# Kernel tuning notes

Measured on AMD Instinct MI355X. Metric: run time of the kernel, lower is better.

Reference implementation:

```python
import jax, jax.numpy as jnp
import numpy as np

B, T, C, HS = 64, 256, 2048, 128


def setup_inputs() -> dict:
    key = jax.random.key(0)
    k1, k2, k3, k4 = jax.random.split(key, 4)
    x = jax.random.normal(k1, (B, T, C), dtype=jnp.float32)
    # Dense(head_size, use_bias=False) kernels, scaled like glorot-ish init
    Wk = jax.random.normal(k2, (C, HS), dtype=jnp.float32) * (C ** -0.5)
    Wq = jax.random.normal(k3, (C, HS), dtype=jnp.float32) * (C ** -0.5)
    Wv = jax.random.normal(k4, (C, HS), dtype=jnp.float32) * (C ** -0.5)
    return {"x": x, "Wk": Wk, "Wq": Wq, "Wv": Wv}


def reference(x, Wk, Wq, Wv):
    Bn, Tn, Cn = x.shape
    k = jnp.einsum("btc,ch->bth", x, Wk)
    q = jnp.einsum("btc,ch->bth", x, Wq)
    v = jnp.einsum("btc,ch->bth", x, Wv)
    # faithful to source: scores = k @ q^T, scaled by C**-0.5 (input dim!)
    scores = jnp.einsum("bth,bsh->bts", k, q) * (Cn ** -0.5)
    causal = jnp.tril(jnp.ones((Tn, Tn), dtype=bool))  # [T, T]
    scores = jnp.where(causal, scores, -jnp.inf)
    weights = jax.nn.softmax(scores, axis=-1)
    return jnp.einsum("bts,bsh->bth", weights, v)
```

## Files before the change

### kernel.cpp

```cpp
#include <hip/hip_runtime.h>
#include <hip/hip_bf16.h>
#include <cstdint>
#include <cstddef>

#define B_  64
#define T_  256
#define C_  2048
#define HS_ 128
#define N_  384

typedef __bf16 bf16x8 __attribute__((ext_vector_type(8)));
typedef float  floatx4 __attribute__((ext_vector_type(4)));

__device__ __forceinline__ unsigned short f2bf_rne(float f) {
  union { float f; unsigned int u; } v; v.f = f;
  unsigned int r = v.u + 0x7fffu + ((v.u >> 16) & 1u);
  return (unsigned short)(r >> 16);
}
__device__ __forceinline__ unsigned short f2bf(float f) {
  union { float f; unsigned int u; } v; v.f = f;
  return (unsigned short)((v.u + 0x8000u) >> 16);
}

__device__ __forceinline__ void async_copy16(const void* g, void* l) {
  __builtin_amdgcn_global_load_lds(
      (const __attribute__((address_space(1))) unsigned int*)g,
      (__attribute__((address_space(3))) unsigned int*)l, 16, 0, 0);
}

__global__ __launch_bounds__(256) void wt_kernel(
    const float* __restrict__ Wk, const float* __restrict__ Wq,
    const float* __restrict__ Wv, unsigned short* __restrict__ Wt) {
  __shared__ float tile[32][33];
  const int w  = blockIdx.z;
  const int c0 = blockIdx.x * 32;
  const int h0 = blockIdx.y * 32;
  const float* W = (w == 0) ? Wk : (w == 1) ? Wq : Wv;
  const int tx = threadIdx.x & 31, ty = threadIdx.x >> 5;
#pragma unroll
  for (int i = 0; i < 32; i += 8)
    tile[ty + i][tx] = W[(size_t)(c0 + ty + i) * HS_ + h0 + tx];
  __syncthreads();
#pragma unroll
  for (int i = 0; i < 32; i += 8) {
    int hh = ty + i, cc = tx;
    Wt[(size_t)(w * HS_ + h0 + hh) * C_ + c0 + cc] = f2bf_rne(tile[cc][hh]);
  }
}

__global__ __launch_bounds__(256, 2) void qkv_gemm(
    const float* __restrict__ X, const unsigned short* __restrict__ Wt,
    unsigned short* __restrict__ kqv, unsigned short* __restrict__ vT) {
  __shared__ unsigned short As[2][128 * 72];
  __shared__ unsigned short Bs[2][96 * 64];

  const int tid  = threadIdx.x;
  const int wave = tid >> 6, lane = tid & 63;
  const int quad = lane >> 4, l16 = lane & 15;

  const int bid = blockIdx.x;
  const int m0  = (bid & 127) * 128;
  const int n0  = (bid >> 7) * 96;
  const int wm  = (wave >> 1) * 64;
  const int wn  = (wave & 1) * 48;

  int bsrc_n[3], bsrc_c[3], bdst[3];
#pragma unroll
  for (int r = 0; r < 3; ++r) {
    int slot = r * 256 + tid;
    int n = slot >> 3, sl = slot & 7;
    bsrc_n[r] = n; bsrc_c[r] = sl ^ (n & 7);
    bdst[r] = (r * 256 + wave * 64) * 8;
  }

  const int arow = tid >> 4;
  const int achk = tid & 15;

#pragma unroll
  for (int r = 0; r < 3; ++r)
    async_copy16(Wt + (size_t)(n0 + bsrc_n[r]) * C_ + bsrc_c[r] * 8,
                 &Bs[0][bdst[r]]);
  float4 av[8];
#pragma unroll
  for (int r = 0; r < 8; ++r)
    av[r] = *(const float4*)(X + (size_t)(m0 + arow + r * 16) * C_ + achk * 4);

  floatx4 acc[4][3] = {};

  for (int k = 0; k < 32; ++k) {
    const int cur = k & 1, nxt = cur ^ 1;
#pragma unroll
    for (int r = 0; r < 8; ++r) {
      ushort4 b4;
      b4.x = f2bf(av[r].x); b4.y = f2bf(av[r].y);
      b4.z = f2bf(av[r].z); b4.w = f2bf(av[r].w);
      *(ushort4*)&As[cur][(arow + r * 16) * 72 + achk * 4] = b4;
    }
    __syncthreads();

    if (k < 31) {
      const int kn = (k + 1) * 64;
#pragma unroll
      for (int r = 0; r < 3; ++r)
        async_copy16(Wt + (size_t)(n0 + bsrc_n[r]) * C_ + kn + bsrc_c[r] * 8,
                     &Bs[nxt][bdst[r]]);
#pragma unroll
      for (int r = 0; r < 8; ++r)
        av[r] = *(const float4*)(X + (size_t)(m0 + arow + r * 16) * C_ + kn + achk * 4);
    }

#pragma unroll
    for (int ks = 0; ks < 2; ++ks) {
      bf16x8 af[4], bfv[3];
#pragma unroll
      for (int mt = 0; mt < 4; ++mt)
        af[mt] = *(const bf16x8*)&As[cur][(wm + mt * 16 + l16) * 72 + ks * 32 + quad * 8];
#pragma unroll
      for (int nt = 0; nt < 3; ++nt) {
        int n = wn + nt * 16 + l16;
        int c = ks * 4 + quad;
        bfv[nt] = *(const bf16x8*)&Bs[cur][n * 64 + (c ^ (n & 7)) * 8];
      }
#pragma unroll
      for (int mt = 0; mt < 4; ++mt)
#pragma unroll
        for (int nt = 0; nt < 3; ++nt)
          acc[mt][nt] = __builtin_amdgcn_mfma_f32_16x16x32_bf16(
              af[mt], bfv[nt], acc[mt][nt], 0, 0, 0);
    }
  }

#pragma unroll
  for (int mt = 0; mt < 4; ++mt)
#pragma unroll
    for (int nt = 0; nt < 3; ++nt)
#pragma unroll
      for (int r = 0; r < 4; ++r) {
        int row = m0 + wm + mt * 16 + quad * 4 + r;
        int col = n0 + wn + nt * 16 + l16;
        unsigned short us = f2bf(acc[mt][nt][r]);
        kqv[(size_t)row * N_ + col] = us;
        if (col >= 256) {
          int bb = row >> 8, tt = row & 255;
          vT[(size_t)bb * HS_ * T_ + (size_t)(col - 256) * T_ + tt] = us;
        }
      }
}

__global__ __launch_bounds__(256) void attn_kernel(
    const unsigned short* __restrict__ kqv, const unsigned short* __restrict__ vT,
    float* __restrict__ out) {
  __shared__ unsigned short P[4][16 * 136];
  __shared__ float Olds[2][16][132];
  __shared__ float rs1[2][16];

  const int tid  = threadIdx.x;
  const int wave = tid >> 6, lane = tid & 63;
  const int quad = lane >> 4, l16 = lane & 15;
  const int tile = wave >> 1, par = wave & 1;
  const int tt = tile ? (15 - (int)blockIdx.x) : (int)blockIdx.x;
  const int b  = blockIdx.y;
  const int t0 = tt * 16;
  const float scale = 0.022097086912079612f;
  const unsigned short* kq = kqv + (size_t)b * T_ * N_;

  bf16x8 kf[4];
#pragma unroll
  for (int ks = 0; ks < 4; ++ks)
    kf[ks] = *(const bf16x8*)&kq[(size_t)(t0 + l16) * N_ + ks * 32 + quad * 8];

  const int n_my = ((tt + 1) + (1 - par)) >> 1;
  const int npad = (n_my + 1) & ~1;

  float rsum[4] = {0.f, 0.f, 0.f, 0.f};

  bf16x8 qf[4];
  if (n_my > 0) {
    const int st = par;
#pragma unroll
    for (int ks = 0; ks < 4; ++ks)
      qf[ks] = *(const bf16x8*)&kq[(size_t)(st * 16 + l16) * N_ + HS_ + ks * 32 + quad * 8];
  }
  for (int j = 0; j < n_my; ++j) {
    bf16x8 qn[4];
    if (j + 1 < n_my) {
      const int st = par + 2 * (j + 1);
#pragma unroll
      for (int ks = 0; ks < 4; ++ks)
        qn[ks] = *(const bf16x8*)&kq[(size_t)(st * 16 + l16) * N_ + HS_ + ks * 32 + quad * 8];
    }
    floatx4 a = {};
#pragma unroll
    for (int ks = 0; ks < 4; ++ks)
      a = __builtin_amdgcn_mfma_f32_16x16x32_bf16(kf[ks], qf[ks], a, 0, 0, 0);
    const int st = par + 2 * j;
    const int scol = st * 16 + l16;
#pragma unroll
    for (int r = 0; r < 4; ++r) {
      int trow = t0 + quad * 4 + r;
      float p = (scol <= trow) ? __expf(a[r] * scale) : 0.f;
      rsum[r] += p;
      P[wave][(quad * 4 + r) * 136 + j * 16 + l16] = f2bf(p);
    }
#pragma unroll
    for (int ks = 0; ks < 4; ++ks) qf[ks] = qn[ks];
  }
  if (npad > n_my) {
#pragma unroll
    for (int r = 0; r < 4; ++r)
      P[wave][(quad * 4 + r) * 136 + n_my * 16 + l16] = 0;
  }
#pragma unroll
  for (int m = 1; m < 16; m <<= 1)
#pragma unroll
    for (int r = 0; r < 4; ++r)
      rsum[r] += __shfl_xor(rsum[r], m, 64);

  floatx4 oacc[8] = {};
  const unsigned short* vb = vT + (size_t)b * HS_ * T_;
  const int nks = npad >> 1;
  const int sb_off = (quad >> 1);
  const int sb_lo  = (quad & 1) * 8;
  bf16x8 bv[8]; bf16x8 pa;
  if (nks > 0) {
    int st = par + 2 * (0 + sb_off);
    int sbase = st * 16 + sb_lo;
    pa = *(const bf16x8*)&P[wave][l16 * 136 + 0 * 32 + quad * 8];
#pragma unroll
    for (int nt = 0; nt < 8; ++nt)
      bv[nt] = *(const bf16x8*)&vb[(size_t)(nt * 16 + l16) * T_ + sbase];
  }
  for (int ks2 = 0; ks2 < nks; ++ks2) {
    bf16x8 bvn[8]; bf16x8 pan;
    if (ks2 + 1 < nks) {
      int jt = 2 * (ks2 + 1) + sb_off;
      int st = par + 2 * jt;
      int sbase = st * 16 + sb_lo;
      pan = *(const bf16x8*)&P[wave][l16 * 136 + (ks2 + 1) * 32 + quad * 8];
#pragma unroll
      for (int nt = 0; nt < 8; ++nt)
        bvn[nt] = *(const bf16x8*)&vb[(size_t)(nt * 16 + l16) * T_ + sbase];
    }
#pragma unroll
    for (int nt = 0; nt < 8; ++nt)
      oacc[nt] = __builtin_amdgcn_mfma_f32_16x16x32_bf16(pa, bv[nt], oacc[nt], 0, 0, 0);
    pa = pan;
#pragma unroll
    for (int nt = 0; nt < 8; ++nt) bv[nt] = bvn[nt];
  }

  if (par == 1) {
#pragma unroll
    for (int nt = 0; nt < 8; ++nt)
#pragma unroll
      for (int r = 0; r < 4; ++r)
        Olds[tile][quad * 4 + r][nt * 16 + l16] = oacc[nt][r];
    if (l16 == 0) {
#pragma unroll
      for (int r = 0; r < 4; ++r) rs1[tile][quad * 4 + r] = rsum[r];
    }
  }
  __syncthreads();
  if (par == 0) {
    float inv[4];
#pragma unroll
    for (int r = 0; r < 4; ++r)
      inv[r] = 1.f / (rsum[r] + rs1[tile][quad * 4 + r]);
    float* ob = out + ((size_t)b * T_ + t0) * HS_;
#pragma unroll
    for (int nt = 0; nt < 8; ++nt)
#pragma unroll
      for (int r = 0; r < 4; ++r) {
        int row = quad * 4 + r;
        ob[(size_t)row * HS_ + nt * 16 + l16] =
            (oacc[nt][r] + Olds[tile][row][nt * 16 + l16]) * inv[r];
      }
  }
}

extern "C" void kernel_launch(void* const* d_in, const int* in_sizes, int n_in,
                              void* d_out, int out_size, void* d_ws, size_t ws_size,
                              hipStream_t stream) {
  const float* x  = (const float*)d_in[0];
  const float* Wk = (const float*)d_in[1];
  const float* Wq = (const float*)d_in[2];
  const float* Wv = (const float*)d_in[3];
  float* out = (float*)d_out;

  char* ws = (char*)d_ws;
  unsigned short* Wt  = (unsigned short*)(ws);
  unsigned short* kqv = (unsigned short*)(ws + 1572864);
  unsigned short* vT  = (unsigned short*)(ws + 1572864 + 12582912);

  hipLaunchKernelGGL(wt_kernel, dim3(64, 4, 3), dim3(256), 0, stream, Wk, Wq, Wv, Wt);
  hipLaunchKernelGGL(qkv_gemm, dim3(512), dim3(256), 0, stream, x, Wt, kqv, vT);
  hipLaunchKernelGGL(attn_kernel, dim3(8, 64), dim3(256), 0, stream, kqv, vT, out);
}
```

Before: 241.8 us.

## Retile QKV GEMM to full-N 32-row blocks and split attention keys four ways

The QKV projection now gives each block 32 rows of x and all 384 output columns, with a K step of 32. Each x element is therefore read and converted to bf16 only once, where before it was read once per N tile. The cost is more B-tile traffic per block and a longer K loop with more barriers. The attention kernel now runs one query tile per block, with its four waves splitting the key tiles four ways and reducing partial outputs through shared memory; the explicit register prefetch of Q and V is dropped, which trades latency hiding for a simpler loop and a better-balanced grid.

```diff
diff --git a/kernel.cpp b/kernel.cpp
--- a/kernel.cpp
+++ b/kernel.cpp
@@ -51,93 +51,79 @@
 __global__ __launch_bounds__(256, 2) void qkv_gemm(
     const float* __restrict__ X, const unsigned short* __restrict__ Wt,
     unsigned short* __restrict__ kqv, unsigned short* __restrict__ vT) {
-  __shared__ unsigned short As[2][128 * 72];
-  __shared__ unsigned short Bs[2][96 * 64];
+  __shared__ unsigned short As[2][32 * 40];
+  __shared__ unsigned short Bs[2][384 * 32];
 
   const int tid  = threadIdx.x;
   const int wave = tid >> 6, lane = tid & 63;
   const int quad = lane >> 4, l16 = lane & 15;
 
-  const int bid = blockIdx.x;
-  const int m0  = (bid & 127) * 128;
-  const int n0  = (bid >> 7) * 96;
-  const int wm  = (wave >> 1) * 64;
-  const int wn  = (wave & 1) * 48;
-
-  int bsrc_n[3], bsrc_c[3], bdst[3];
-#pragma unroll
-  for (int r = 0; r < 3; ++r) {
-    int slot = r * 256 + tid;
-    int n = slot >> 3, sl = slot & 7;
-    bsrc_n[r] = n; bsrc_c[r] = sl ^ (n & 7);
+  const int m0 = blockIdx.x * 32;
+  const int wn = wave * 96;
+
+  int bn[6], bc[6], bdst[6];
+#pragma unroll
+  for (int r = 0; r < 6; ++r) {
+    int s = r * 256 + tid;
+    int n = s >> 2, c = s & 3;
+    bn[r] = n; bc[r] = c ^ (n & 3);
     bdst[r] = (r * 256 + wave * 64) * 8;
   }
 
-  const int arow = tid >> 4;
-  const int achk = tid & 15;
-
-#pragma unroll
-  for (int r = 0; r < 3; ++r)
-    async_copy16(Wt + (size_t)(n0 + bsrc_n[r]) * C_ + bsrc_c[r] * 8,
-                 &Bs[0][bdst[r]]);
-  float4 av[8];
-#pragma unroll
-  for (int r = 0; r < 8; ++r)
-    av[r] = *(const float4*)(X + (size_t)(m0 + arow + r * 16) * C_ + achk * 4);
-
-  floatx4 acc[4][3] = {};
-
-  for (int k = 0; k < 32; ++k) {
+  const int arow = tid >> 3;
+  const int achk = tid & 7;
+
+#pragma unroll
+  for (int r = 0; r < 6; ++r)
+    async_copy16(Wt + (size_t)bn[r] * C_ + bc[r] * 8, &Bs[0][bdst[r]]);
+  float4 av = *(const float4*)(X + (size_t)(m0 + arow) * C_ + achk * 4);
+
+  floatx4 acc[2][6] = {};
+
+  for (int k = 0; k < 64; ++k) {
     const int cur = k & 1, nxt = cur ^ 1;
-#pragma unroll
-    for (int r = 0; r < 8; ++r) {
+    {
       ushort4 b4;
-      b4.x = f2bf(av[r].x); b4.y = f2bf(av[r].y);
-      b4.z = f2bf(av[r].z); b4.w = f2bf(av[r].w);
-      *(ushort4*)&As[cur][(arow + r * 16) * 72 + achk * 4] = b4;
+      b4.x = f2bf(av.x); b4.y = f2bf(av.y);
+      b4.z = f2bf(av.z); b4.w = f2bf(av.w);
+      *(ushort4*)&As[cur][arow * 40 + achk * 4] = b4;
     }
     __syncthreads();
 
-    if (k < 31) {
-      const int kn = (k + 1) * 64;
-#pragma unroll
-      for (int r = 0; r < 3; ++r)
-        async_copy16(Wt + (size_t)(n0 + bsrc_n[r]) * C_ + kn + bsrc_c[r] * 8,
-                     &Bs[nxt][bdst[r]]);
-#pragma unroll
-      for (int r = 0; r < 8; ++r)
-        av[r] = *(const float4*)(X + (size_t)(m0 + arow + r * 16) * C_ + kn + achk * 4);
-    }
-
-#pragma unroll
-    for (int ks = 0; ks < 2; ++ks) {
-      bf16x8 af[4], bfv[3];
-#pragma unroll
-      for (int mt = 0; mt < 4; ++mt)
-        af[mt] = *(const bf16x8*)&As[cur][(wm + mt * 16 + l16) * 72 + ks * 32 + quad * 8];
-#pragma unroll
-      for (int nt = 0; nt < 3; ++nt) {
-        int n = wn + nt * 16 + l16;
-        int c = ks * 4 + quad;
-        bfv[nt] = *(const bf16x8*)&Bs[cur][n * 64 + (c ^ (n & 7)) * 8];
-      }
-#pragma unroll
-      for (int mt = 0; mt < 4; ++mt)
-#pragma unroll
-        for (int nt = 0; nt < 3; ++nt)
-          acc[mt][nt] = __builtin_amdgcn_mfma_f32_16x16x32_bf16(
-              af[mt], bfv[nt], acc[mt][nt], 0, 0, 0);
-    }
-  }
-
-#pragma unroll
-  for (int mt = 0; mt < 4; ++mt)
-#pragma unroll
-    for (int nt = 0; nt < 3; ++nt)
+    if (k < 63) {
+      const int kn = (k + 1) * 32;
+#pragma unroll
+      for (int r = 0; r < 6; ++r)
+        async_copy16(Wt + (size_t)bn[r] * C_ + kn + bc[r] * 8, &Bs[nxt][bdst[r]]);
+      av = *(const float4*)(X + (size_t)(m0 + arow) * C_ + kn + achk * 4);
+    }
+
+    bf16x8 af[2], bfv[6];
+#pragma unroll
+    for (int mt = 0; mt < 2; ++mt)
+      af[mt] = *(const bf16x8*)&As[cur][(mt * 16 + l16) * 40 + quad * 8];
+#pragma unroll
+    for (int nt = 0; nt < 6; ++nt) {
+      int n = wn + nt * 16 + l16;
+      int c = quad ^ (n & 3);
+      bfv[nt] = *(const bf16x8*)&Bs[cur][n * 32 + c * 8];
+    }
+#pragma unroll
+    for (int mt = 0; mt < 2; ++mt)
+#pragma unroll
+      for (int nt = 0; nt < 6; ++nt)
+        acc[mt][nt] = __builtin_amdgcn_mfma_f32_16x16x32_bf16(
+            af[mt], bfv[nt], acc[mt][nt], 0, 0, 0);
+  }
+
+#pragma unroll
+  for (int mt = 0; mt < 2; ++mt)
+#pragma unroll
+    for (int nt = 0; nt < 6; ++nt)
 #pragma unroll
       for (int r = 0; r < 4; ++r) {
-        int row = m0 + wm + mt * 16 + quad * 4 + r;
-        int col = n0 + wn + nt * 16 + l16;
+        int row = m0 + mt * 16 + quad * 4 + r;
+        int col = wn + nt * 16 + l16;
         unsigned short us = f2bf(acc[mt][nt][r]);
         kqv[(size_t)row * N_ + col] = us;
         if (col >= 256) {
@@ -150,15 +136,15 @@
 __global__ __launch_bounds__(256) void attn_kernel(
     const unsigned short* __restrict__ kqv, const unsigned short* __restrict__ vT,
     float* __restrict__ out) {
-  __shared__ unsigned short P[4][16 * 136];
-  __shared__ float Olds[2][16][132];
-  __shared__ float rs1[2][16];
+  __shared__ unsigned short P[4][16 * 72];
+  __shared__ float Olds[3][16][132];
+  __shared__ float rs1[3][16];
 
   const int tid  = threadIdx.x;
-  const int wave = tid >> 6, lane = tid & 63;
+  const int par  = tid >> 6;
+  const int lane = tid & 63;
   const int quad = lane >> 4, l16 = lane & 15;
-  const int tile = wave >> 1, par = wave & 1;
-  const int tt = tile ? (15 - (int)blockIdx.x) : (int)blockIdx.x;
+  const int tt = blockIdx.x;
   const int b  = blockIdx.y;
   const int t0 = tt * 16;
   const float scale = 0.022097086912079612f;
@@ -169,46 +155,34 @@
   for (int ks = 0; ks < 4; ++ks)
     kf[ks] = *(const bf16x8*)&kq[(size_t)(t0 + l16) * N_ + ks * 32 + quad * 8];
 
-  const int n_my = ((tt + 1) + (1 - par)) >> 1;
+  const int n_my = (tt >= par) ? (((tt - par) >> 2) + 1) : 0;
   const int npad = (n_my + 1) & ~1;
 
   float rsum[4] = {0.f, 0.f, 0.f, 0.f};
 
-  bf16x8 qf[4];
-  if (n_my > 0) {
-    const int st = par;
+  for (int j = 0; j < n_my; ++j) {
+    const int st = par + 4 * j;
+    bf16x8 qf[4];
 #pragma unroll
     for (int ks = 0; ks < 4; ++ks)
       qf[ks] = *(const bf16x8*)&kq[(size_t)(st * 16 + l16) * N_ + HS_ + ks * 32 + quad * 8];
-  }
-  for (int j = 0; j < n_my; ++j) {
-    bf16x8 qn[4];
-    if (j + 1 < n_my) {
-      const int st = par + 2 * (j + 1);
-#pragma unroll
-      for (int ks = 0; ks < 4; ++ks)
-        qn[ks] = *(const bf16x8*)&kq[(size_t)(st * 16 + l16) * N_ + HS_ + ks * 32 + quad * 8];
-    }
     floatx4 a = {};
 #pragma unroll
     for (int ks = 0; ks < 4; ++ks)
       a = __builtin_amdgcn_mfma_f32_16x16x32_bf16(kf[ks], qf[ks], a, 0, 0, 0);
-    const int st = par + 2 * j;
     const int scol = st * 16 + l16;
 #pragma unroll
     for (int r = 0; r < 4; ++r) {
       int trow = t0 + quad * 4 + r;
       float p = (scol <= trow) ? __expf(a[r] * scale) : 0.f;
       rsum[r] += p;
-      P[wave][(quad * 4 + r) * 136 + j * 16 + l16] = f2bf(p);
-    }
-#pragma unroll
-    for (int ks = 0; ks < 4; ++ks) qf[ks] = qn[ks];
+      P[par][(quad * 4 + r) * 72 + j * 16 + l16] = f2bf(p);
+    }
   }
   if (npad > n_my) {
 #pragma unroll
     for (int r = 0; r < 4; ++r)
-      P[wave][(quad * 4 + r) * 136 + n_my * 16 + l16] = 0;
+      P[par][(quad * 4 + r) * 72 + n_my * 16 + l16] = 0;
   }
 #pragma unroll
   for (int m = 1; m < 16; m <<= 1)
@@ -221,59 +195,46 @@
   const int nks = npad >> 1;
   const int sb_off = (quad >> 1);
   const int sb_lo  = (quad & 1) * 8;
-  bf16x8 bv[8]; bf16x8 pa;
-  if (nks > 0) {
-    int st = par + 2 * (0 + sb_off);
-    int sbase = st * 16 + sb_lo;
-    pa = *(const bf16x8*)&P[wave][l16 * 136 + 0 * 32 + quad * 8];
+  for (int ks2 = 0; ks2 < nks; ++ks2) {
+    const int jt = 2 * ks2 + sb_off;
+    const int st = par + 4 * jt;
+    const int sbase = st * 16 + sb_lo;
+    bf16x8 pa = *(const bf16x8*)&P[par][l16 * 72 + ks2 * 32 + quad * 8];
+#pragma unroll
+    for (int nt = 0; nt < 8; ++nt) {
+      bf16x8 bv = *(const bf16x8*)&vb[(size_t)(nt * 16 + l16) * T_ + sbase];
+      oacc[nt] = __builtin_amdgcn_mfma_f32_16x16x32_bf16(pa, bv, oacc[nt], 0, 0, 0);
+    }
+  }
+
+  if (par > 0) {
 #pragma unroll
     for (int nt = 0; nt < 8; ++nt)
-      bv[nt] = *(const bf16x8*)&vb[(size_t)(nt * 16 + l16) * T_ + sbase];
-  }
-  for (int ks2 = 0; ks2 < nks; ++ks2) {
-    bf16x8 bvn[8]; bf16x8 pan;
-    if (ks2 + 1 < nks) {
-      int jt = 2 * (ks2 + 1) + sb_off;
-      int st = par + 2 * jt;
-      int sbase = st * 16 + sb_lo;
-      pan = *(const bf16x8*)&P[wave][l16 * 136 + (ks2 + 1) * 32 + quad * 8];
-#pragma unroll
-      for (int nt = 0; nt < 8; ++nt)
-        bvn[nt] = *(const bf16x8*)&vb[(size_t)(nt * 16 + l16) * T_ + sbase];
-    }
-#pragma unroll
-    for (int nt = 0; nt < 8; ++nt)
-      oacc[nt] = __builtin_amdgcn_mfma_f32_16x16x32_bf16(pa, bv[nt], oacc[nt], 0, 0, 0);
-    pa = pan;
-#pragma unroll
-    for (int nt = 0; nt < 8; ++nt) bv[nt] = bvn[nt];
-  }
-
-  if (par == 1) {
-#pragma unroll
-    for (int nt = 0; nt < 8; ++nt)
 #pragma unroll
       for (int r = 0; r < 4; ++r)
-        Olds[tile][quad * 4 + r][nt * 16 + l16] = oacc[nt][r];
+        Olds[par - 1][quad * 4 + r][nt * 16 + l16] = oacc[nt][r];
     if (l16 == 0) {
 #pragma unroll
-      for (int r = 0; r < 4; ++r) rs1[tile][quad * 4 + r] = rsum[r];
+      for (int r = 0; r < 4; ++r) rs1[par - 1][quad * 4 + r] = rsum[r];
     }
   }
   __syncthreads();
   if (par == 0) {
     float inv[4];
 #pragma unroll
-    for (int r = 0; r < 4; ++r)
-      inv[r] = 1.f / (rsum[r] + rs1[tile][quad * 4 + r]);
+    for (int r = 0; r < 4; ++r) {
+      int row = quad * 4 + r;
+      inv[r] = 1.f / (rsum[r] + rs1[0][row] + rs1[1][row] + rs1[2][row]);
+    }
     float* ob = out + ((size_t)b * T_ + t0) * HS_;
 #pragma unroll
     for (int nt = 0; nt < 8; ++nt)
 #pragma unroll
       for (int r = 0; r < 4; ++r) {
         int row = quad * 4 + r;
-        ob[(size_t)row * HS_ + nt * 16 + l16] =
-            (oacc[nt][r] + Olds[tile][row][nt * 16 + l16]) * inv[r];
+        int col = nt * 16 + l16;
+        ob[(size_t)row * HS_ + col] =
+            (oacc[nt][r] + Olds[0][row][col] + Olds[1][row][col] + Olds[2][row][col]) * inv[r];
       }
   }
 }
@@ -294,5 +255,5 @@
 
   hipLaunchKernelGGL(wt_kernel, dim3(64, 4, 3), dim3(256), 0, stream, Wk, Wq, Wv, Wt);
   hipLaunchKernelGGL(qkv_gemm, dim3(512), dim3(256), 0, stream, x, Wt, kqv, vT);
-  hipLaunchKernelGGL(attn_kernel, dim3(8, 64), dim3(256), 0, stream, kqv, vT, out);
-}
+  hipLaunchKernelGGL(attn_kernel, dim3(16, 64), dim3(256), 0, stream, kqv, vT, out);
+}
```

Result: slower. 290.2 us (+20.0%).

## Restructure QKV GEMM tiling to 64x192 with register-staged double-buffered prefetch

Applied to the files above, without the earlier changes.

The QKV projection GEMM moves from 128x96 tiles to 64x192 tiles, so every block covers two of the three weight matrices' columns. The async global-to-LDS copies for the weights are replaced by register prefetch, with two k-steps of A and B kept in flight. The A tile also gets an XOR-swizzled LDS layout, and a hand-written lgkmcnt wait plus barrier replaces __syncthreads. This aims to hide global load latency and cut LDS bank conflicts, at the cost of more registers per thread and possible occupancy loss.

```diff
diff --git a/kernel.cpp b/kernel.cpp
--- a/kernel.cpp
+++ b/kernel.cpp
@@ -20,12 +20,6 @@
 __device__ __forceinline__ unsigned short f2bf(float f) {
   union { float f; unsigned int u; } v; v.f = f;
   return (unsigned short)((v.u + 0x8000u) >> 16);
-}
-
-__device__ __forceinline__ void async_copy16(const void* g, void* l) {
-  __builtin_amdgcn_global_load_lds(
-      (const __attribute__((address_space(1))) unsigned int*)g,
-      (__attribute__((address_space(3))) unsigned int*)l, 16, 0, 0);
 }
 
 __global__ __launch_bounds__(256) void wt_kernel(
@@ -51,89 +45,113 @@
 __global__ __launch_bounds__(256, 2) void qkv_gemm(
     const float* __restrict__ X, const unsigned short* __restrict__ Wt,
     unsigned short* __restrict__ kqv, unsigned short* __restrict__ vT) {
-  __shared__ unsigned short As[2][128 * 72];
-  __shared__ unsigned short Bs[2][96 * 64];
+  __shared__ unsigned short As[2][64 * 64];
+  __shared__ unsigned short Bs[2][192 * 64];
 
   const int tid  = threadIdx.x;
   const int wave = tid >> 6, lane = tid & 63;
   const int quad = lane >> 4, l16 = lane & 15;
 
   const int bid = blockIdx.x;
-  const int m0  = (bid & 127) * 128;
-  const int n0  = (bid >> 7) * 96;
-  const int wm  = (wave >> 1) * 64;
-  const int wn  = (wave & 1) * 48;
-
-  int bsrc_n[3], bsrc_c[3], bdst[3];
-#pragma unroll
-  for (int r = 0; r < 3; ++r) {
-    int slot = r * 256 + tid;
-    int n = slot >> 3, sl = slot & 7;
-    bsrc_n[r] = n; bsrc_c[r] = sl ^ (n & 7);
-    bdst[r] = (r * 256 + wave * 64) * 8;
-  }
-
-  const int arow = tid >> 4;
-  const int achk = tid & 15;
-
-#pragma unroll
-  for (int r = 0; r < 3; ++r)
-    async_copy16(Wt + (size_t)(n0 + bsrc_n[r]) * C_ + bsrc_c[r] * 8,
-                 &Bs[0][bdst[r]]);
-  float4 av[8];
-#pragma unroll
-  for (int r = 0; r < 8; ++r)
-    av[r] = *(const float4*)(X + (size_t)(m0 + arow + r * 16) * C_ + achk * 4);
-
-  floatx4 acc[4][3] = {};
-
-  for (int k = 0; k < 32; ++k) {
-    const int cur = k & 1, nxt = cur ^ 1;
-#pragma unroll
-    for (int r = 0; r < 8; ++r) {
-      ushort4 b4;
-      b4.x = f2bf(av[r].x); b4.y = f2bf(av[r].y);
-      b4.z = f2bf(av[r].z); b4.w = f2bf(av[r].w);
-      *(ushort4*)&As[cur][(arow + r * 16) * 72 + achk * 4] = b4;
-    }
-    __syncthreads();
-
-    if (k < 31) {
-      const int kn = (k + 1) * 64;
-#pragma unroll
-      for (int r = 0; r < 3; ++r)
-        async_copy16(Wt + (size_t)(n0 + bsrc_n[r]) * C_ + kn + bsrc_c[r] * 8,
-                     &Bs[nxt][bdst[r]]);
-#pragma unroll
-      for (int r = 0; r < 8; ++r)
-        av[r] = *(const float4*)(X + (size_t)(m0 + arow + r * 16) * C_ + kn + achk * 4);
-    }
-
-#pragma unroll
-    for (int ks = 0; ks < 2; ++ks) {
-      bf16x8 af[4], bfv[3];
-#pragma unroll
-      for (int mt = 0; mt < 4; ++mt)
-        af[mt] = *(const bf16x8*)&As[cur][(wm + mt * 16 + l16) * 72 + ks * 32 + quad * 8];
-#pragma unroll
-      for (int nt = 0; nt < 3; ++nt) {
-        int n = wn + nt * 16 + l16;
-        int c = ks * 4 + quad;
-        bfv[nt] = *(const bf16x8*)&Bs[cur][n * 64 + (c ^ (n & 7)) * 8];
-      }
-#pragma unroll
-      for (int mt = 0; mt < 4; ++mt)
-#pragma unroll
-        for (int nt = 0; nt < 3; ++nt)
-          acc[mt][nt] = __builtin_amdgcn_mfma_f32_16x16x32_bf16(
-              af[mt], bfv[nt], acc[mt][nt], 0, 0, 0);
-    }
-  }
-
-#pragma unroll
-  for (int mt = 0; mt < 4; ++mt)
-#pragma unroll
-    for (int nt = 0; nt < 3; ++nt)
+  const int m0  = (bid & 255) * 64;
+  const int n0  = (bid >> 8) * 192;
+  const int wm  = (wave >> 1) * 32;
+  const int wn  = (wave & 1) * 96;
+
+  int arow[4], achk[4], aoff[4];
+#pragma unroll
+  for (int r = 0; r < 4; ++r) {
+    int s = r * 256 + tid;
+    arow[r] = s >> 4; achk[r] = s & 15;
+    aoff[r] = arow[r] * 64 + (((achk[r] >> 1) ^ (arow[r] & 7)) << 3) + ((achk[r] & 1) << 2);
+  }
+  int bn[6], bc[6], boff[6];
+#pragma unroll
+  for (int r = 0; r < 6; ++r) {
+    int s = r * 256 + tid;
+    bn[r] = s >> 3; bc[r] = s & 7;
+    boff[r] = bn[r] * 64 + ((bc[r] ^ (bn[r] & 7)) << 3);
+  }
+
+#define LOAD_A(AV, KN)                                                         \
+  {                                                                            \
+    _Pragma("unroll")                                                          \
+    for (int r = 0; r < 4; ++r)                                                \
+      AV[r] = *(const float4*)(X + (size_t)(m0 + arow[r]) * C_ + (KN) + achk[r] * 4); \
+  }
+#define LOAD_B(BV, KN)                                                         \
+  {                                                                            \
+    _Pragma("unroll")                                                          \
+    for (int r = 0; r < 6; ++r)                                                \
+      BV[r] = *(const uint4*)(Wt + (size_t)(n0 + bn[r]) * C_ + (KN) + bc[r] * 8); \
+  }
+#define STAGE(AV, BV, BUF)                                                     \
+  {                                                                            \
+    _Pragma("unroll")                                                          \
+    for (int r = 0; r < 4; ++r) {                                              \
+      ushort4 b4;                                                              \
+      b4.x = f2bf(AV[r].x); b4.y = f2bf(AV[r].y);                              \
+      b4.z = f2bf(AV[r].z); b4.w = f2bf(AV[r].w);                              \
+      *(ushort4*)&As[BUF][aoff[r]] = b4;                                       \
+    }                                                                          \
+    _Pragma("unroll")                                                          \
+    for (int r = 0; r < 6; ++r)                                                \
+      *(uint4*)&Bs[BUF][boff[r]] = BV[r];                                      \
+  }
+#define BARRIER() asm volatile("s_waitcnt lgkmcnt(0)\n\ts_barrier" ::: "memory")
+#define COMPUTE(BUF)                                                           \
+  {                                                                            \
+    _Pragma("unroll")                                                          \
+    for (int ks = 0; ks < 2; ++ks) {                                           \
+      bf16x8 af[2], bfv[6];                                                    \
+      _Pragma("unroll")                                                        \
+      for (int mt = 0; mt < 2; ++mt) {                                         \
+        int row = wm + mt * 16 + l16;                                          \
+        int c = ks * 4 + quad;                                                 \
+        af[mt] = *(const bf16x8*)&As[BUF][row * 64 + ((c ^ (row & 7)) << 3)];  \
+      }                                                                        \
+      _Pragma("unroll")                                                        \
+      for (int nt = 0; nt < 6; ++nt) {                                         \
+        int n = wn + nt * 16 + l16;                                            \
+        int c = ks * 4 + quad;                                                 \
+        bfv[nt] = *(const bf16x8*)&Bs[BUF][n * 64 + ((c ^ (n & 7)) << 3)];     \
+      }                                                                        \
+      _Pragma("unroll")                                                        \
+      for (int mt = 0; mt < 2; ++mt)                                           \
+        _Pragma("unroll")                                                      \
+        for (int nt = 0; nt < 6; ++nt)                                         \
+          acc[mt][nt] = __builtin_amdgcn_mfma_f32_16x16x32_bf16(               \
+              af[mt], bfv[nt], acc[mt][nt], 0, 0, 0);                          \
+    }                                                                          \
+  }
+
+  float4 a0[4], a1[4]; uint4 b0[6], b1[6];
+  LOAD_A(a0, 0); LOAD_B(b0, 0);
+  LOAD_A(a1, 64); LOAD_B(b1, 64);
+
+  floatx4 acc[2][6] = {};
+
+  for (int k2 = 0; k2 < 16; ++k2) {
+    const int k = k2 * 2;
+    STAGE(a0, b0, 0);
+    BARRIER();
+    if (k2 < 15) { LOAD_A(a0, (k + 2) * 64); LOAD_B(b0, (k + 2) * 64); }
+    COMPUTE(0);
+    STAGE(a1, b1, 1);
+    BARRIER();
+    if (k2 < 15) { LOAD_A(a1, (k + 3) * 64); LOAD_B(b1, (k + 3) * 64); }
+    COMPUTE(1);
+  }
+#undef LOAD_A
+#undef LOAD_B
+#undef STAGE
+#undef BARRIER
+#undef COMPUTE
+
+#pragma unroll
+  for (int mt = 0; mt < 2; ++mt)
+#pragma unroll
+    for (int nt = 0; nt < 6; ++nt)
 #pragma unroll
       for (int r = 0; r < 4; ++r) {
         int row = m0 + wm + mt * 16 + quad * 4 + r;
```

Result: slower. 339.7 us (+40.5%).

## Shrink QKV GEMM M-tile to 64, swizzle A smem, group blocks for reuse

Applied to the files above, without the earlier changes.

Halves the QKV projection GEMM M tile from 128 to 64 rows, doubling the grid to 1024 blocks and raising the launch-bounds occupancy target from 2 to 4 blocks per CU. The A tile in shared memory drops its padding in favour of an XOR swizzle, which shrinks LDS use. Block indices are remapped so groups of 8 M-tiles share the same N-block, which should improve L2 reuse of the weight slices. The aim is better latency hiding and load balance across CUs, at the cost of each block reusing its weight tile over fewer rows and doing fewer MFMAs per load.

```diff
diff --git a/kernel.cpp b/kernel.cpp
--- a/kernel.cpp
+++ b/kernel.cpp
@@ -48,53 +48,59 @@
   }
 }
 
-__global__ __launch_bounds__(256, 2) void qkv_gemm(
+__global__ __launch_bounds__(256, 4) void qkv_gemm(
     const float* __restrict__ X, const unsigned short* __restrict__ Wt,
     unsigned short* __restrict__ kqv, unsigned short* __restrict__ vT) {
-  __shared__ unsigned short As[2][128 * 72];
+  __shared__ unsigned short As[2][64 * 64];
   __shared__ unsigned short Bs[2][96 * 64];
 
   const int tid  = threadIdx.x;
   const int wave = tid >> 6, lane = tid & 63;
   const int quad = lane >> 4, l16 = lane & 15;
 
-  const int bid = blockIdx.x;
-  const int m0  = (bid & 127) * 128;
-  const int n0  = (bid >> 7) * 96;
-  const int wm  = (wave >> 1) * 64;
-  const int wn  = (wave & 1) * 48;
-
-  int bsrc_n[3], bsrc_c[3], bdst[3];
+  const int g  = blockIdx.x;
+  const int ml = g & 7;
+  const int nb = (g >> 3) & 3;
+  const int mh = g >> 5;
+  const int m0 = (mh * 8 + ml) * 64;
+  const int n0 = nb * 96;
+  const int wm = (wave >> 1) * 32;
+  const int wn = (wave & 1) * 48;
+
+  const unsigned short* bsrc[3]; int bdst[3];
 #pragma unroll
   for (int r = 0; r < 3; ++r) {
-    int slot = r * 256 + tid;
-    int n = slot >> 3, sl = slot & 7;
-    bsrc_n[r] = n; bsrc_c[r] = sl ^ (n & 7);
+    int s = r * 256 + tid;
+    int n = s >> 3, sl = s & 7;
+    bsrc[r] = Wt + (size_t)(n0 + n) * C_ + (sl ^ (n & 7)) * 8;
     bdst[r] = (r * 256 + wave * 64) * 8;
   }
-
-  const int arow = tid >> 4;
-  const int achk = tid & 15;
+  int arow[4], achk[4], awoff[4];
+#pragma unroll
+  for (int r = 0; r < 4; ++r) {
+    int s = r * 256 + tid;
+    arow[r] = s >> 4; achk[r] = s & 15;
+    awoff[r] = arow[r] * 64 + (((achk[r] >> 1) ^ (arow[r] & 7)) << 3) + ((achk[r] & 1) << 2);
+  }
 
 #pragma unroll
   for (int r = 0; r < 3; ++r)
-    async_copy16(Wt + (size_t)(n0 + bsrc_n[r]) * C_ + bsrc_c[r] * 8,
-                 &Bs[0][bdst[r]]);
-  float4 av[8];
-#pragma unroll
-  for (int r = 0; r < 8; ++r)
-    av[r] = *(const float4*)(X + (size_t)(m0 + arow + r * 16) * C_ + achk * 4);
-
-  floatx4 acc[4][3] = {};
+    async_copy16(bsrc[r], &Bs[0][bdst[r]]);
+  float4 av[4];
+#pragma unroll
+  for (int r = 0; r < 4; ++r)
+    av[r] = *(const float4*)(X + (size_t)(m0 + arow[r]) * C_ + achk[r] * 4);
+
+  floatx4 acc[2][3] = {};
 
   for (int k = 0; k < 32; ++k) {
     const int cur = k & 1, nxt = cur ^ 1;
 #pragma unroll
-    for (int r = 0; r < 8; ++r) {
+    for (int r = 0; r < 4; ++r) {
       ushort4 b4;
       b4.x = f2bf(av[r].x); b4.y = f2bf(av[r].y);
       b4.z = f2bf(av[r].z); b4.w = f2bf(av[r].w);
-      *(ushort4*)&As[cur][(arow + r * 16) * 72 + achk * 4] = b4;
+      *(ushort4*)&As[cur][awoff[r]] = b4;
     }
     __syncthreads();
 
@@ -102,27 +108,27 @@
       const int kn = (k + 1) * 64;
 #pragma unroll
       for (int r = 0; r < 3; ++r)
-        async_copy16(Wt + (size_t)(n0 + bsrc_n[r]) * C_ + kn + bsrc_c[r] * 8,
-                     &Bs[nxt][bdst[r]]);
-#pragma unroll
-      for (int r = 0; r < 8; ++r)
-        av[r] = *(const float4*)(X + (size_t)(m0 + arow + r * 16) * C_ + kn + achk * 4);
+        async_copy16(bsrc[r] + kn, &Bs[nxt][bdst[r]]);
+#pragma unroll
+      for (int r = 0; r < 4; ++r)
+        av[r] = *(const float4*)(X + (size_t)(m0 + arow[r]) * C_ + kn + achk[r] * 4);
     }
 
 #pragma unroll
     for (int ks = 0; ks < 2; ++ks) {
-      bf16x8 af[4], bfv[3];
-#pragma unroll
-      for (int mt = 0; mt < 4; ++mt)
-        af[mt] = *(const bf16x8*)&As[cur][(wm + mt * 16 + l16) * 72 + ks * 32 + quad * 8];
+      bf16x8 af[2], bfv[3];
+#pragma unroll
+      for (int mt = 0; mt < 2; ++mt) {
+        int rr = wm + mt * 16 + l16;
+        af[mt] = *(const bf16x8*)&As[cur][rr * 64 + (((ks * 4 + quad) ^ (rr & 7)) << 3)];
+      }
 #pragma unroll
       for (int nt = 0; nt < 3; ++nt) {
         int n = wn + nt * 16 + l16;
-        int c = ks * 4 + quad;
-        bfv[nt] = *(const bf16x8*)&Bs[cur][n * 64 + (c ^ (n & 7)) * 8];
+        bfv[nt] = *(const bf16x8*)&Bs[cur][n * 64 + (((ks * 4 + quad) ^ (n & 7)) << 3)];
       }
 #pragma unroll
-      for (int mt = 0; mt < 4; ++mt)
+      for (int mt = 0; mt < 2; ++mt)
 #pragma unroll
         for (int nt = 0; nt < 3; ++nt)
           acc[mt][nt] = __builtin_amdgcn_mfma_f32_16x16x32_bf16(
@@ -131,7 +137,7 @@
   }
 
 #pragma unroll
-  for (int mt = 0; mt < 4; ++mt)
+  for (int mt = 0; mt < 2; ++mt)
 #pragma unroll
     for (int nt = 0; nt < 3; ++nt)
 #pragma unroll
@@ -293,6 +299,6 @@
   unsigned short* vT  = (unsigned short*)(ws + 1572864 + 12582912);
 
   hipLaunchKernelGGL(wt_kernel, dim3(64, 4, 3), dim3(256), 0, stream, Wk, Wq, Wv, Wt);
-  hipLaunchKernelGGL(qkv_gemm, dim3(512), dim3(256), 0, stream, x, Wt, kqv, vT);
+  hipLaunchKernelGGL(qkv_gemm, dim3(1024), dim3(256), 0, stream, x, Wt, kqv, vT);
   hipLaunchKernelGGL(attn_kernel, dim3(8, 64), dim3(256), 0, stream, kqv, vT, out);
 }
```

After: 247.9 us. +2.5%, slower.
